# Kernel optimization log

Measured on AMD Instinct MI355X. Metric: run time of the kernel, lower is better.

The kernel has to match this reference:

```python
import jax, jax.numpy as jnp
import numpy as np

B, N_WIN, N, C = 32, 64, 64, 256          # batch, windows/img, tokens/window, dim
Wh, Ww = 8, 8                              # window_size
H_RES, W_RES = 64, 64                      # input_resolution
NUM_HEADS = 1


def _relative_coords():
    coords = np.stack(np.meshgrid(np.arange(Wh), np.arange(Ww), indexing='ij')).reshape(2, -1)
    rel = coords[:, :, None] - coords[:, None, :]   # [2, N, N]
    return rel[0].astype(np.int32), rel[1].astype(np.int32)  # radius, azimuth


def setup_inputs() -> dict:
    key = jax.random.key(0)
    ks = jax.random.split(key, 10)
    B_ = B * N_WIN
    radius_np, azimuth_np = _relative_coords()
    std = 0.02
    return {
        'x': jax.random.normal(ks[0], (B_, N, C), dtype=jnp.float32),
        'theta_max': jax.random.uniform(ks[1], (B,), dtype=jnp.float32) * np.float32(np.pi),
        'qkv_w': jax.random.normal(ks[2], (3 * C, C), dtype=jnp.float32) * std,
        'qkv_b': jnp.zeros((3 * C,), dtype=jnp.float32),
        'proj_w': jax.random.normal(ks[3], (C, C), dtype=jnp.float32) * std,
        'proj_b': jnp.zeros((C,), dtype=jnp.float32),
        'a_p': jax.random.normal(ks[4], (2 * Ww - 1, NUM_HEADS), dtype=jnp.float32) * std,
        'b_p': jax.random.normal(ks[5], (2 * Ww - 1, NUM_HEADS), dtype=jnp.float32) * std,
        'a_r': jax.random.normal(ks[6], (2 * Wh - 1, NUM_HEADS), dtype=jnp.float32) * std,
        'b_r': jax.random.normal(ks[7], (2 * Wh - 1, NUM_HEADS), dtype=jnp.float32) * std,
        'radius': jnp.asarray(radius_np),
        'azimuth': jnp.asarray(azimuth_np),
    }


def reference(x, theta_max, qkv_w, qkv_b, proj_w, proj_b, a_p, b_p, a_r, b_r, radius, azimuth):
    B_, n, c = x.shape
    head_dim = c // NUM_HEADS
    scale = head_dim ** -0.5

    qkv = (x @ qkv_w.T + qkv_b).reshape(B_, n, 3, NUM_HEADS, head_dim).transpose(2, 0, 3, 1, 4)
    q, k, v = qkv[0], qkv[1], qkv[2]            # each [B_, h, N, d]
    attn = jnp.einsum('bhnd,bhmd->bhnm', q * scale, k)

    # polar azimuth bias (torch negative-index wrap on the table)
    Tp = a_p.shape[0]
    aidx = jnp.where(azimuth < 0, azimuth + Tp, azimuth)
    azf = azimuth.astype(x.dtype) * (2.0 * np.pi / W_RES)        # [N, N]
    A_phi = a_p[aidx] * jnp.cos(azf)[..., None] + b_p[aidx] * jnp.sin(azf)[..., None]  # [N, N, h]
    bias_phi = jnp.transpose(A_phi, (2, 0, 1))[None]             # [1, h, N, N]

    # polar radius bias, modulated per-sample by theta_max
    Tr = a_r.shape[0]
    ridx = jnp.where(radius < 0, radius + Tr, radius)
    nW = B_ // theta_max.shape[0]
    tm = jnp.repeat(theta_max, nW).reshape(B_, 1, 1, 1)
    rnew = radius.astype(x.dtype)[None, :, :, None] * tm / H_RES  # [B_, N, N, 1]
    A_r = a_r[ridx][None] * jnp.cos(rnew) + b_r[ridx][None] * jnp.sin(rnew)  # [B_, N, N, h]
    A_theta = jnp.transpose(A_r, (0, 3, 1, 2))                   # [B_, h, N, N]

    attn = jax.nn.softmax(attn + bias_phi + A_theta, axis=-1)
    out = jnp.einsum('bhnm,bhmd->bhnd', attn, v).transpose(0, 2, 1, 3).reshape(B_, n, c)
    return out @ proj_w.T + proj_b
```

## Files before the change

### kernel.cpp

```cpp
#include <hip/hip_runtime.h>
#include <stdint.h>

#define NWINDOWS 2048

typedef short bf16x8 __attribute__((ext_vector_type(8)));
typedef float f32x4  __attribute__((ext_vector_type(4)));

#define OFF_WQKV  0u
#define OFF_WPROJ 393216u
#define OFF_BQKV  524288u
#define OFF_BIAS  527360u
#define OFF_QKV   1051648u
#define WS_NEED   202378240u

__device__ __forceinline__ unsigned short f2bf(float f) {
    union { float f; unsigned int u; } v; v.f = f;
    unsigned int u = v.u;
    u += 0x7FFFu + ((u >> 16) & 1u);
    return (unsigned short)(u >> 16);
}

__global__ __launch_bounds__(256)
void prep_kernel(const float* __restrict__ qkv_w, const float* __restrict__ qkv_b,
                 const float* __restrict__ proj_w, const float* __restrict__ theta_max,
                 const float* __restrict__ a_p, const float* __restrict__ b_p,
                 const float* __restrict__ a_r, const float* __restrict__ b_r,
                 const int* __restrict__ radius, const int* __restrict__ azimuth,
                 unsigned short* __restrict__ w_qkv, unsigned short* __restrict__ w_proj,
                 float* __restrict__ b_qkv, float* __restrict__ bias_tbl)
{
    int idx = blockIdx.x * 256 + threadIdx.x;
    const float scale = 0.0625f;
    if (idx < 196608) {
        int row = idx >> 8;
        float v = qkv_w[idx];
        if (row < 256) v *= scale;
        w_qkv[idx] = f2bf(v);
    } else if (idx < 196608 + 65536) {
        int j = idx - 196608;
        w_proj[j] = f2bf(proj_w[j]);
    } else if (idx < 196608 + 65536 + 768) {
        int j = idx - (196608 + 65536);
        float v = qkv_b[j];
        if (j < 256) v *= scale;
        b_qkv[j] = v;
    } else if (idx < 196608 + 65536 + 768 + 131072) {
        int j = idx - (196608 + 65536 + 768);
        int b  = j >> 12;
        int ij = j & 4095;
        int az = azimuth[ij];
        int rd = radius[ij];
        int aidx = az < 0 ? az + 15 : az;
        int ridx = rd < 0 ? rd + 15 : rd;
        float azf = (float)az * 0.09817477042468103f;
        float phi = a_p[aidx] * cosf(azf) + b_p[aidx] * sinf(azf);
        float rn  = (float)rd * theta_max[b] * 0.015625f;
        bias_tbl[j] = phi + a_r[ridx] * cosf(rn) + b_r[ridx] * sinf(rn);
    }
}

__global__ __launch_bounds__(256, 2)
void qkv_gemm(const float* __restrict__ x, const unsigned short* __restrict__ w_qkv,
              const float* __restrict__ b_qkv, unsigned short* __restrict__ qkv)
{
    __shared__ unsigned short Cst[4 * 64 * 136];

    const int w    = threadIdx.x >> 6;
    const int lane = threadIdx.x & 63;
    const int quad = lane >> 4;
    const int l16  = lane & 15;
    const int mbase = blockIdx.x * 256 + w * 64;
    unsigned short* cw = Cst + w * (64 * 136);

    bf16x8 af[4][8];
    #pragma unroll
    for (int rt = 0; rt < 4; ++rt) {
        const float* xrow = x + (size_t)(mbase + rt * 16 + l16) * 256;
        #pragma unroll
        for (int kk = 0; kk < 8; ++kk) {
            const float4* p = (const float4*)(xrow + kk * 32 + quad * 8);
            float4 v0 = p[0], v1 = p[1];
            bf16x8 a;
            a[0] = (short)f2bf(v0.x); a[1] = (short)f2bf(v0.y);
            a[2] = (short)f2bf(v0.z); a[3] = (short)f2bf(v0.w);
            a[4] = (short)f2bf(v1.x); a[5] = (short)f2bf(v1.y);
            a[6] = (short)f2bf(v1.z); a[7] = (short)f2bf(v1.w);
            af[rt][kk] = a;
        }
    }

    auto loadB = [&](bf16x8 (&b)[8], int nt) {
        const unsigned short* wp = w_qkv + (nt * 16 + l16) * 256 + quad * 8;
        #pragma unroll
        for (int kk = 0; kk < 8; ++kk)
            b[kk] = *(const bf16x8*)(wp + kk * 32);
    };

    auto tile = [&](const bf16x8 (&b)[8], int nt) {
        int ncol = nt * 16 + l16;
        float bias = b_qkv[ncol];
        f32x4 acc[4] = {{0,0,0,0},{0,0,0,0},{0,0,0,0},{0,0,0,0}};
        #pragma unroll
        for (int kk = 0; kk < 8; ++kk)
            #pragma unroll
            for (int rt = 0; rt < 4; ++rt)
                acc[rt] = __builtin_amdgcn_mfma_f32_16x16x32_bf16(af[rt][kk], b[kk], acc[rt], 0, 0, 0);
        int tcol = (nt & 7) * 16 + l16;
        #pragma unroll
        for (int rt = 0; rt < 4; ++rt)
            #pragma unroll
            for (int r = 0; r < 4; ++r) {
                int row  = rt * 16 + quad * 4 + r;
                int colp = tcol ^ (((row >> 3) & 1) << 4);
                cw[row * 136 + colp] = f2bf(acc[rt][r] + bias);
            }
    };

    auto flushC = [&](int group) {
        int colbase = group * 128;
        int rowg  = lane >> 4;
        int chunk = lane & 15;
        #pragma unroll
        for (int i = 0; i < 16; ++i) {
            int row = i * 4 + rowg;
            int cs  = chunk ^ (((row >> 3) & 1) << 1);
            bf16x8 v = *(const bf16x8*)(cw + row * 136 + cs * 8);
            *(bf16x8*)(qkv + (size_t)(mbase + row) * 768 + colbase + chunk * 8) = v;
        }
    };

    bf16x8 b0[8], b1[8];
    loadB(b0, 0);
    for (int nt = 0; nt < 48; nt += 2) {
        loadB(b1, nt + 1);
        tile(b0, nt);
        if (nt + 2 < 48) loadB(b0, nt + 2);
        tile(b1, nt + 1);
        if ((nt & 7) == 6) flushC(nt >> 3);
    }
}

__global__ __launch_bounds__(256, 2)
void attn_proj(const float* __restrict__ bias_tbl, const unsigned short* __restrict__ qkv,
               const unsigned short* __restrict__ w_proj, const float* __restrict__ proj_b,
               float* __restrict__ out)
{
    __shared__ unsigned short vT[256 * 64];
    __shared__ unsigned short Pl[64 * 72];
    __shared__ unsigned short Ol[64 * 264];

    const int win   = blockIdx.x;
    const int batch = win >> 6;
    const size_t rowbase = (size_t)win * 64;
    const int tid  = threadIdx.x;
    const int w    = tid >> 6;
    const int lane = tid & 63;
    const int quad = lane >> 4;
    const int l16  = lane & 15;

    {
        int tok  = tid >> 2;
        int part = tid & 3;
        const unsigned short* src = qkv + (rowbase + tok) * 768 + 512;
        #pragma unroll
        for (int jc = 0; jc < 8; ++jc) {
            int c = jc * 4 + part;
            bf16x8 v8 = *(const bf16x8*)(src + c * 8);
            #pragma unroll
            for (int e = 0; e < 8; ++e) {
                int d   = c * 8 + e;
                int swz = (((tok >> 3) ^ (d & 7)) << 3) | (tok & 7);
                vT[d * 64 + swz] = (unsigned short)v8[e];
            }
        }
    }

    bf16x8 qf[8];
    const unsigned short* qrow = qkv + (rowbase + w * 16 + l16) * 768;
    #pragma unroll
    for (int kk = 0; kk < 8; ++kk)
        qf[kk] = *(const bf16x8*)(qrow + kk * 32 + quad * 8);

    f32x4 S[4];
    #pragma unroll
    for (int t = 0; t < 4; ++t) {
        const unsigned short* krow = qkv + (rowbase + t * 16 + l16) * 768 + 256 + quad * 8;
        f32x4 c = {0.f, 0.f, 0.f, 0.f};
        #pragma unroll
        for (int kk = 0; kk < 8; ++kk) {
            bf16x8 b = *(const bf16x8*)(krow + kk * 32);
            c = __builtin_amdgcn_mfma_f32_16x16x32_bf16(qf[kk], b, c, 0, 0, 0);
        }
        S[t] = c;
    }

    const float* bt = bias_tbl + batch * 4096 + (w * 16 + quad * 4) * 64 + l16;
    #pragma unroll
    for (int t = 0; t < 4; ++t)
        #pragma unroll
        for (int r = 0; r < 4; ++r)
            S[t][r] += bt[r * 64 + t * 16];

    float inv[4];
    #pragma unroll
    for (int r = 0; r < 4; ++r) {
        float m = fmaxf(fmaxf(S[0][r], S[1][r]), fmaxf(S[2][r], S[3][r]));
        #pragma unroll
        for (int off = 1; off < 16; off <<= 1)
            m = fmaxf(m, __shfl_xor(m, off, 64));
        float s = 0.f;
        #pragma unroll
        for (int t = 0; t < 4; ++t) { S[t][r] = __expf(S[t][r] - m); s += S[t][r]; }
        #pragma unroll
        for (int off = 1; off < 16; off <<= 1)
            s += __shfl_xor(s, off, 64);
        inv[r] = 1.0f / s;
    }

    #pragma unroll
    for (int t = 0; t < 4; ++t)
        #pragma unroll
        for (int r = 0; r < 4; ++r)
            Pl[(w * 16 + quad * 4 + r) * 72 + t * 16 + l16] = f2bf(S[t][r] * inv[r]);

    __syncthreads();

    #pragma unroll
    for (int n = 0; n < 16; ++n) {
        f32x4 c = {0.f, 0.f, 0.f, 0.f};
        int dim = n * 16 + l16;
        #pragma unroll
        for (int kk = 0; kk < 2; ++kk) {
            bf16x8 a = *(const bf16x8*)(&Pl[(w * 16 + l16) * 72 + kk * 32 + quad * 8]);
            int chunk = (kk * 4 + quad) ^ (dim & 7);
            bf16x8 b = *(const bf16x8*)(&vT[dim * 64 + chunk * 8]);
            c = __builtin_amdgcn_mfma_f32_16x16x32_bf16(a, b, c, 0, 0, 0);
        }
        #pragma unroll
        for (int r = 0; r < 4; ++r)
            Ol[(w * 16 + quad * 4 + r) * 264 + dim] = f2bf(c[r]);
    }

    __syncthreads();

    bf16x8 af[4][8];
    #pragma unroll
    for (int rt = 0; rt < 4; ++rt)
        #pragma unroll
        for (int kk = 0; kk < 8; ++kk)
            af[rt][kk] = *(const bf16x8*)(&Ol[(rt * 16 + l16) * 264 + kk * 32 + quad * 8]);

    #pragma unroll
    for (int ntl = 0; ntl < 4; ++ntl) {
        int ncol = w * 64 + ntl * 16 + l16;
        const unsigned short* wp = w_proj + ncol * 256 + quad * 8;
        f32x4 acc[4] = {{0,0,0,0},{0,0,0,0},{0,0,0,0},{0,0,0,0}};
        #pragma unroll
        for (int kk = 0; kk < 8; ++kk) {
            bf16x8 b = *(const bf16x8*)(wp + kk * 32);
            #pragma unroll
            for (int rt = 0; rt < 4; ++rt)
                acc[rt] = __builtin_amdgcn_mfma_f32_16x16x32_bf16(af[rt][kk], b, acc[rt], 0, 0, 0);
        }
        float pb = proj_b[ncol];
        #pragma unroll
        for (int rt = 0; rt < 4; ++rt)
            #pragma unroll
            for (int r = 0; r < 4; ++r)
                out[(rowbase + rt * 16 + quad * 4 + r) * 256 + ncol] = acc[rt][r] + pb;
    }
}

extern "C" void kernel_launch(void* const* d_in, const int* in_sizes, int n_in,
                              void* d_out, int out_size, void* d_ws, size_t ws_size,
                              hipStream_t stream)
{
    const float* x       = (const float*)d_in[0];
    const float* theta   = (const float*)d_in[1];
    const float* qkv_w   = (const float*)d_in[2];
    const float* qkv_b   = (const float*)d_in[3];
    const float* proj_w  = (const float*)d_in[4];
    const float* proj_b  = (const float*)d_in[5];
    const float* a_p     = (const float*)d_in[6];
    const float* b_p     = (const float*)d_in[7];
    const float* a_r     = (const float*)d_in[8];
    const float* b_r     = (const float*)d_in[9];
    const int*   radius  = (const int*)d_in[10];
    const int*   azimuth = (const int*)d_in[11];

    if (ws_size < (size_t)WS_NEED) return;

    char* ws = (char*)d_ws;
    unsigned short* w_qkv    = (unsigned short*)(ws + OFF_WQKV);
    unsigned short* w_proj   = (unsigned short*)(ws + OFF_WPROJ);
    float*          b_qkv    = (float*)(ws + OFF_BQKV);
    float*          bias_tbl = (float*)(ws + OFF_BIAS);
    unsigned short* qkv      = (unsigned short*)(ws + OFF_QKV);

    prep_kernel<<<1540, 256, 0, stream>>>(qkv_w, qkv_b, proj_w, theta,
                                          a_p, b_p, a_r, b_r, radius, azimuth,
                                          w_qkv, w_proj, b_qkv, bias_tbl);
    qkv_gemm<<<512, 256, 0, stream>>>(x, w_qkv, b_qkv, qkv);
    attn_proj<<<NWINDOWS, 256, 0, stream>>>(bias_tbl, qkv, w_proj, proj_b, (float*)d_out);
}
```

Measured before the change: 443.2 us.

## Stage QKV weight tiles in LDS via async global-to-LDS loads with smaller M tiles

The QKV GEMM drops from 64 to 32 rows per wave (128 per block) and doubles the grid. Each B tile is now loaded once per block into a swizzled, double-buffered LDS buffer with global_load_lds, instead of every wave loading it from global memory into registers. The aim is to cut redundant weight traffic and register pressure so four blocks fit per CU. In exchange it adds a block-wide barrier every N-tile and does half as much MFMA work per loaded A fragment.

```diff
diff --git a/kernel.cpp b/kernel.cpp
--- a/kernel.cpp
+++ b/kernel.cpp
@@ -59,22 +59,24 @@
     }
 }
 
-__global__ __launch_bounds__(256, 2)
+__global__ __launch_bounds__(256, 4)
 void qkv_gemm(const float* __restrict__ x, const unsigned short* __restrict__ w_qkv,
               const float* __restrict__ b_qkv, unsigned short* __restrict__ qkv)
 {
-    __shared__ unsigned short Cst[4 * 64 * 136];
-
-    const int w    = threadIdx.x >> 6;
-    const int lane = threadIdx.x & 63;
+    __shared__ __align__(16) unsigned short Bs[2][16 * 256];
+    __shared__ __align__(16) unsigned short Cp[4][32 * 72];
+
+    const int tid  = threadIdx.x;
+    const int w    = tid >> 6;
+    const int lane = tid & 63;
     const int quad = lane >> 4;
     const int l16  = lane & 15;
-    const int mbase = blockIdx.x * 256 + w * 64;
-    unsigned short* cw = Cst + w * (64 * 136);
-
-    bf16x8 af[4][8];
-    #pragma unroll
-    for (int rt = 0; rt < 4; ++rt) {
+    const int m3   = l16 & 7;
+    const int mbase = blockIdx.x * 128 + w * 32;
+
+    bf16x8 af[2][8];
+    #pragma unroll
+    for (int rt = 0; rt < 2; ++rt) {
         const float* xrow = x + (size_t)(mbase + rt * 16 + l16) * 256;
         #pragma unroll
         for (int kk = 0; kk < 8; ++kk) {
@@ -89,54 +91,61 @@
         }
     }
 
-    auto loadB = [&](bf16x8 (&b)[8], int nt) {
-        const unsigned short* wp = w_qkv + (nt * 16 + l16) * 256 + quad * 8;
-        #pragma unroll
-        for (int kk = 0; kk < 8; ++kk)
-            b[kk] = *(const bf16x8*)(wp + kk * 32);
+    const int srow = tid >> 5;
+    const int sc   = (tid & 31) ^ ((srow & 7) << 2);
+    unsigned short* const db[2] = { &Bs[0][w * 512], &Bs[1][w * 512] };
+
+    auto stage = [&](int nt, int buf) {
+        const unsigned short* s0 = w_qkv + (nt * 16 + srow) * 256 + sc * 8;
+        unsigned short* d = db[buf];
+        __builtin_amdgcn_global_load_lds(
+            (const __attribute__((address_space(1))) void*)s0,
+            (__attribute__((address_space(3))) void*)d, 16, 0, 0);
+        __builtin_amdgcn_global_load_lds(
+            (const __attribute__((address_space(1))) void*)(s0 + 8 * 256),
+            (__attribute__((address_space(3))) void*)(d + 2048), 16, 0, 0);
     };
 
-    auto tile = [&](const bf16x8 (&b)[8], int nt) {
-        int ncol = nt * 16 + l16;
-        float bias = b_qkv[ncol];
-        f32x4 acc[4] = {{0,0,0,0},{0,0,0,0},{0,0,0,0},{0,0,0,0}};
-        #pragma unroll
-        for (int kk = 0; kk < 8; ++kk)
+    stage(0, 0);
+    __syncthreads();
+
+    const int rdoff = l16 * 256 + quad * 8;
+    unsigned short* const cw = &Cp[w][0];
+    const int frow = lane >> 3;
+    const int fch  = lane & 7;
+
+    for (int nt = 0; nt < 48; ++nt) {
+        const int buf = nt & 1;
+        if (nt + 1 < 48) stage(nt + 1, buf ^ 1);
+
+        f32x4 acc0 = {0.f, 0.f, 0.f, 0.f};
+        f32x4 acc1 = {0.f, 0.f, 0.f, 0.f};
+        const unsigned short* bs = &Bs[buf][0] + rdoff;
+        #pragma unroll
+        for (int kk = 0; kk < 8; ++kk) {
+            bf16x8 b = *(const bf16x8*)(bs + ((kk ^ m3) << 5));
+            acc0 = __builtin_amdgcn_mfma_f32_16x16x32_bf16(af[0][kk], b, acc0, 0, 0, 0);
+            acc1 = __builtin_amdgcn_mfma_f32_16x16x32_bf16(af[1][kk], b, acc1, 0, 0, 0);
+        }
+
+        const float bias = b_qkv[nt * 16 + l16];
+        const int tcol = (nt & 3) * 16 + l16;
+        #pragma unroll
+        for (int r = 0; r < 4; ++r) {
+            cw[(quad * 4 + r) * 72 + tcol]      = f2bf(acc0[r] + bias);
+            cw[(16 + quad * 4 + r) * 72 + tcol] = f2bf(acc1[r] + bias);
+        }
+
+        if ((nt & 3) == 3) {
+            const int colbase = (nt >> 2) * 64;
             #pragma unroll
-            for (int rt = 0; rt < 4; ++rt)
-                acc[rt] = __builtin_amdgcn_mfma_f32_16x16x32_bf16(af[rt][kk], b[kk], acc[rt], 0, 0, 0);
-        int tcol = (nt & 7) * 16 + l16;
-        #pragma unroll
-        for (int rt = 0; rt < 4; ++rt)
-            #pragma unroll
-            for (int r = 0; r < 4; ++r) {
-                int row  = rt * 16 + quad * 4 + r;
-                int colp = tcol ^ (((row >> 3) & 1) << 4);
-                cw[row * 136 + colp] = f2bf(acc[rt][r] + bias);
+            for (int i = 0; i < 4; ++i) {
+                int row = i * 8 + frow;
+                bf16x8 v = *(const bf16x8*)(cw + row * 72 + fch * 8);
+                *(bf16x8*)(qkv + (size_t)(mbase + row) * 768 + colbase + fch * 8) = v;
             }
-    };
-
-    auto flushC = [&](int group) {
-        int colbase = group * 128;
-        int rowg  = lane >> 4;
-        int chunk = lane & 15;
-        #pragma unroll
-        for (int i = 0; i < 16; ++i) {
-            int row = i * 4 + rowg;
-            int cs  = chunk ^ (((row >> 3) & 1) << 1);
-            bf16x8 v = *(const bf16x8*)(cw + row * 136 + cs * 8);
-            *(bf16x8*)(qkv + (size_t)(mbase + row) * 768 + colbase + chunk * 8) = v;
-        }
-    };
-
-    bf16x8 b0[8], b1[8];
-    loadB(b0, 0);
-    for (int nt = 0; nt < 48; nt += 2) {
-        loadB(b1, nt + 1);
-        tile(b0, nt);
-        if (nt + 2 < 48) loadB(b0, nt + 2);
-        tile(b1, nt + 1);
-        if ((nt & 7) == 6) flushC(nt >> 3);
+        }
+        __syncthreads();
     }
 }
 
@@ -300,6 +309,6 @@
     prep_kernel<<<1540, 256, 0, stream>>>(qkv_w, qkv_b, proj_w, theta,
                                           a_p, b_p, a_r, b_r, radius, azimuth,
                                           w_qkv, w_proj, b_qkv, bias_tbl);
-    qkv_gemm<<<512, 256, 0, stream>>>(x, w_qkv, b_qkv, qkv);
+    qkv_gemm<<<1024, 256, 0, stream>>>(x, w_qkv, b_qkv, qkv);
     attn_proj<<<NWINDOWS, 256, 0, stream>>>(bias_tbl, qkv, w_proj, proj_b, (float*)d_out);
 }
```

Measured after the change: 405.4 us. 8.5% less time.
